# Kernel tuning notes

Measured on AMD Instinct MI355X. Metric: run time of the kernel, lower is better.

## Reference

```python
import math
import jax, jax.numpy as jnp
import numpy as np

D = 1024
H = 16
DK = D // H
B = 4
L = 2048


def setup_inputs() -> dict:
    key = jax.random.key(0)
    ks = jax.random.split(key, 11)
    s = 1.0 / math.sqrt(D)
    return {
        "q": jax.random.normal(ks[0], (B, L, D), jnp.float32),
        "k": jax.random.normal(ks[1], (B, L, D), jnp.float32),
        "v": jax.random.normal(ks[2], (B, L, D), jnp.float32),
        "wq_w": jax.random.normal(ks[3], (D, D), jnp.float32) * s,
        "wq_b": jnp.zeros((D,), jnp.float32),
        "wk_w": jax.random.normal(ks[4], (D, D), jnp.float32) * s,
        "wk_b": jnp.zeros((D,), jnp.float32),
        "wv_w": jax.random.normal(ks[5], (D, D), jnp.float32) * s,
        "wv_b": jnp.zeros((D,), jnp.float32),
        "wo_w": jax.random.normal(ks[6], (D, D), jnp.float32) * s,
        "wo_b": jnp.zeros((D,), jnp.float32),
    }


def reference(q, k, v, wq_w, wq_b, wk_w, wk_b, wv_w, wv_b, wo_w, wo_b):
    # torch Linear: x @ W.T + b
    Q = (q @ wq_w.T + wq_b).reshape(B, L, H, DK).transpose(0, 2, 1, 3)  # [B,H,L,DK]
    K = (k @ wk_w.T + wk_b).reshape(B, -1, H, DK).transpose(0, 2, 1, 3)
    V = (v @ wv_w.T + wv_b).reshape(B, -1, H, DK).transpose(0, 2, 1, 3)
    sc = jnp.einsum("bhqd,bhkd->bhqk", Q, K) / math.sqrt(DK)  # [B,H,L,L]
    # causal mask: strictly upper triangular filled with -1e9
    cm = jnp.triu(jnp.ones((L, L), dtype=bool), 1)
    sc = jnp.where(cm, jnp.float32(-1e9), sc)
    at = jax.nn.softmax(sc, axis=-1)  # dropout p=0 (eval)
    out = jnp.einsum("bhqk,bhkd->bhqd", at, V)  # [B,H,L,DK]
    out = out.transpose(0, 2, 1, 3).reshape(B, L, D)
    return out @ wo_w.T + wo_b
```

## Files before the change

kernel.cpp:

```cpp
#include <hip/hip_runtime.h>
#include <stdint.h>

#define DD 1024
#define NH 16
#define DHEAD 64
#define NB 4
#define SEQ 2048
#define MR (NB*SEQ)
#define NT (SEQ/128)

typedef __attribute__((ext_vector_type(8))) short s8v;
typedef __attribute__((ext_vector_type(4))) float f4v;

__device__ __forceinline__ unsigned short f2bf(float f) {
  union { float f; uint32_t u; } c; c.f = f;
  uint32_t u = c.u;
  u += 0x7fffu + ((u >> 16) & 1u);
  return (unsigned short)(u >> 16);
}
__device__ __forceinline__ unsigned short f2bf_trunc(float f) {
  union { float f; uint32_t u; } c; c.f = f;
  return (unsigned short)(c.u >> 16);
}

__device__ __forceinline__ void load_lds16(const void* g, void* lds) {
  __builtin_amdgcn_global_load_lds(
      (__attribute__((address_space(1))) void*)(uintptr_t)g,
      (__attribute__((address_space(3))) void*)(uint32_t)(uintptr_t)lds,
      16, 0, 0);
}

__global__ void cvt_all(
    const float* __restrict__ w0, const float* __restrict__ w1,
    const float* __restrict__ w2, const float* __restrict__ w3,
    const float* __restrict__ a0, const float* __restrict__ a1,
    const float* __restrict__ a2,
    unsigned short* __restrict__ dw0, unsigned short* __restrict__ dw1,
    unsigned short* __restrict__ dw2, unsigned short* __restrict__ dw3,
    unsigned short* __restrict__ da0, unsigned short* __restrict__ da1,
    unsigned short* __restrict__ da2)
{
  int blk = blockIdx.x;
  const float* src;
  unsigned short* dst;
  size_t i;
  if (blk < 2048) {
    int a = blk >> 9;
    src = a == 0 ? w0 : (a == 1 ? w1 : (a == 2 ? w2 : w3));
    dst = a == 0 ? dw0 : (a == 1 ? dw1 : (a == 2 ? dw2 : dw3));
    i = (size_t)(blk & 511) * 2048 + (size_t)threadIdx.x * 8;
  } else {
    int blk2 = blk - 2048;
    int a = blk2 >> 12;
    src = a == 0 ? a0 : (a == 1 ? a1 : a2);
    dst = a == 0 ? da0 : (a == 1 ? da1 : da2);
    i = (size_t)(blk2 & 4095) * 2048 + (size_t)threadIdx.x * 8;
  }
  float4 a4 = *(const float4*)(src + i);
  float4 b4 = *(const float4*)(src + i + 4);
  union { unsigned short us[8]; uint4 u; } t;
  t.us[0] = f2bf(a4.x); t.us[1] = f2bf(a4.y); t.us[2] = f2bf(a4.z); t.us[3] = f2bf(a4.w);
  t.us[4] = f2bf(b4.x); t.us[5] = f2bf(b4.y); t.us[6] = f2bf(b4.z); t.us[7] = f2bf(b4.w);
  *(uint4*)(dst + i) = t.u;
}

__global__ __launch_bounds__(256, 2) void gemm_bt(
    const unsigned short* __restrict__ A,
    const unsigned short* __restrict__ Bw,
    const float* __restrict__ bias,
    float* __restrict__ Cout)
{
  __shared__ __align__(16) short As[128 * 64];
  __shared__ __align__(16) short Bs[128 * 64];
  const int linear = blockIdx.y * 8 + blockIdx.x;
  const int nx = linear >> 6;
  const int my = linear & 63;
  const int tid = threadIdx.x;
  const int wave = tid >> 6, lane = tid & 63;
  const int wm = (wave >> 1) * 64, wn = (wave & 1) * 64;
  const int lr = lane & 15, lg = lane >> 4;
  const int sw = lr & 7;
  const unsigned short* Ab = A + (size_t)my * 128 * DD;
  const unsigned short* Bb = Bw + (size_t)nx * 128 * DD;

  f4v z = {0.f, 0.f, 0.f, 0.f};
  f4v acc[4][4];
  for (int mi = 0; mi < 4; mi++) for (int ni = 0; ni < 4; ni++) acc[mi][ni] = z;

  for (int k0 = 0; k0 < DD; k0 += 64) {
    __syncthreads();
    for (int i = 0; i < 4; i++) {
      int c = tid + i * 256;
      int row = c >> 3, pg = c & 7;
      load_lds16(Ab + (size_t)row * DD + k0 + ((pg ^ (row & 7)) << 3), As + c * 8);
    }
    for (int i = 0; i < 4; i++) {
      int c = tid + i * 256;
      int row = c >> 3, pg = c & 7;
      load_lds16(Bb + (size_t)row * DD + k0 + ((pg ^ (row & 7)) << 3), Bs + c * 8);
    }
    __syncthreads();
    for (int kk = 0; kk < 64; kk += 32) {
      int gb = kk >> 3;
      s8v af[4], bf[4];
      for (int i = 0; i < 4; i++)
        af[i] = *(const s8v*)(As + (wm + i * 16 + lr) * 64 + (((gb + lg) ^ sw) << 3));
      for (int i = 0; i < 4; i++)
        bf[i] = *(const s8v*)(Bs + (wn + i * 16 + lr) * 64 + (((gb + lg) ^ sw) << 3));
      for (int mi = 0; mi < 4; mi++)
        for (int ni = 0; ni < 4; ni++)
          acc[mi][ni] = __builtin_amdgcn_mfma_f32_16x16x32_bf16(af[mi], bf[ni], acc[mi][ni], 0, 0, 0);
    }
  }
  for (int ni = 0; ni < 4; ni++) {
    int col = nx * 128 + wn + ni * 16 + lr;
    float bv = bias[col];
    for (int mi = 0; mi < 4; mi++) {
      int row0 = my * 128 + wm + mi * 16 + lg * 4;
      for (int r = 0; r < 4; r++)
        Cout[(size_t)(row0 + r) * DD + col] = acc[mi][ni][r] + bv;
    }
  }
}

__global__ __launch_bounds__(256, 2) void gemm_qkv(
    const unsigned short* __restrict__ qA, const unsigned short* __restrict__ kA,
    const unsigned short* __restrict__ vA,
    const unsigned short* __restrict__ wq, const unsigned short* __restrict__ wk,
    const unsigned short* __restrict__ wv,
    const float* __restrict__ bq, const float* __restrict__ bk, const float* __restrict__ bv,
    unsigned short* __restrict__ Qp, unsigned short* __restrict__ Kp,
    unsigned short* __restrict__ VpT)
{
  __shared__ __align__(16) short As[128 * 64];
  __shared__ __align__(16) short Bs[128 * 64];
  const int linear = blockIdx.y * 24 + blockIdx.x;
  const int nx  = linear / 192;
  const int rem = linear % 192;
  const int seg = rem >> 6;
  const int my  = rem & 63;
  const unsigned short* A  = seg == 0 ? qA : (seg == 1 ? kA : vA);
  const unsigned short* Bw = seg == 0 ? wq : (seg == 1 ? wk : wv);
  const float* bias        = seg == 0 ? bq : (seg == 1 ? bk : bv);

  const int tid = threadIdx.x;
  const int wave = tid >> 6, lane = tid & 63;
  const int wm = (wave >> 1) * 64, wn = (wave & 1) * 64;
  const int lr = lane & 15, lg = lane >> 4;
  const int sw = lr & 7;
  const unsigned short* Ab = A + (size_t)my * 128 * DD;
  const unsigned short* Bb = Bw + (size_t)nx * 128 * DD;

  f4v z = {0.f, 0.f, 0.f, 0.f};
  f4v acc[4][4];
  for (int mi = 0; mi < 4; mi++) for (int ni = 0; ni < 4; ni++) acc[mi][ni] = z;

  for (int k0 = 0; k0 < DD; k0 += 64) {
    __syncthreads();
    for (int i = 0; i < 4; i++) {
      int c = tid + i * 256;
      int row = c >> 3, pg = c & 7;
      load_lds16(Ab + (size_t)row * DD + k0 + ((pg ^ (row & 7)) << 3), As + c * 8);
    }
    for (int i = 0; i < 4; i++) {
      int c = tid + i * 256;
      int row = c >> 3, pg = c & 7;
      load_lds16(Bb + (size_t)row * DD + k0 + ((pg ^ (row & 7)) << 3), Bs + c * 8);
    }
    __syncthreads();
    for (int kk = 0; kk < 64; kk += 32) {
      int gb = kk >> 3;
      s8v af[4], bf[4];
      for (int i = 0; i < 4; i++)
        af[i] = *(const s8v*)(As + (wm + i * 16 + lr) * 64 + (((gb + lg) ^ sw) << 3));
      for (int i = 0; i < 4; i++)
        bf[i] = *(const s8v*)(Bs + (wn + i * 16 + lr) * 64 + (((gb + lg) ^ sw) << 3));
      for (int mi = 0; mi < 4; mi++)
        for (int ni = 0; ni < 4; ni++)
          acc[mi][ni] = __builtin_amdgcn_mfma_f32_16x16x32_bf16(af[mi], bf[ni], acc[mi][ni], 0, 0, 0);
    }
  }
  if (seg < 2) {
    unsigned short* Cout = seg == 0 ? Qp : Kp;
    for (int ni = 0; ni < 4; ni++) {
      int col = nx * 128 + wn + ni * 16 + lr;
      float bv = bias[col];
      for (int mi = 0; mi < 4; mi++) {
        int row0 = my * 128 + wm + mi * 16 + lg * 4;
        for (int r = 0; r < 4; r++)
          Cout[(size_t)(row0 + r) * DD + col] = f2bf(acc[mi][ni][r] + bv);
      }
    }
  } else {
    for (int ni = 0; ni < 4; ni++) {
      int col = nx * 128 + wn + ni * 16 + lr;
      float bv = bias[col];
      int hh = col >> 6, dd = col & 63;
      for (int mi = 0; mi < 4; mi++) {
        int row0 = my * 128 + wm + mi * 16 + lg * 4;
        int bb = row0 >> 11, ll = row0 & 2047;
        uint64_t w = 0;
        for (int r = 0; r < 4; r++)
          w |= (uint64_t)f2bf(acc[mi][ni][r] + bv) << (16 * r);
        *(uint64_t*)(VpT + ((size_t)(bb * NH + hh) * 64 + dd) * SEQ + ll) = w;
      }
    }
  }
}

#define KS_STRIDE 72
#define VT_STRIDE 136
#define PS_STRIDE 72

__device__ __forceinline__ void attn_step(
    const s8v (&qf)[2][2], const s8v (&kf)[2][4],
    f4v (&o)[2][4], float (&ls)[2][4],
    int qbase, int colbase,
    const short* __restrict__ Vt, int vsub, short* __restrict__ Pw,
    int lr, int lg)
{
  const float csc = 0.125f * 1.44269504089f;
  const float FM = 14.0f;
  f4v zv = {0.f, 0.f, 0.f, 0.f};
  f4v s[2][4];
  for (int mi = 0; mi < 2; mi++) for (int ni = 0; ni < 4; ni++) s[mi][ni] = zv;
  __builtin_amdgcn_s_setprio(1);
  for (int ks = 0; ks < 2; ks++)
    for (int mi = 0; mi < 2; mi++)
      for (int ni = 0; ni < 4; ni++)
        s[mi][ni] = __builtin_amdgcn_mfma_f32_16x16x32_bf16(qf[mi][ks], kf[ks][ni], s[mi][ni], 0, 0, 0);
  __builtin_amdgcn_s_setprio(0);
  const bool diag = (colbase + 63 > qbase);
  for (int mi = 0; mi < 2; mi++)
    for (int ni = 0; ni < 4; ni++)
      for (int r = 0; r < 4; r++) {
        float e = __builtin_amdgcn_exp2f(fmaf(s[mi][ni][r], csc, -FM));
        if (diag) {
          int row = qbase + mi * 16 + lg * 4 + r;
          int col = colbase + ni * 16 + lr;
          e = (col > row) ? 0.f : e;
        }
        ls[mi][r] += e;
        Pw[(mi * 16 + lg * 4 + r) * PS_STRIDE + ni * 16 + lr] = (short)f2bf_trunc(e);
      }
  for (int kc2 = 0; kc2 < 2; kc2++) {
    s8v pf[2], vf[4];
    for (int mi = 0; mi < 2; mi++)
      pf[mi] = *(const s8v*)(Pw + (mi * 16 + lr) * PS_STRIDE + kc2 * 32 + lg * 8);
    for (int ni = 0; ni < 4; ni++)
      vf[ni] = *(const s8v*)(Vt + (ni * 16 + lr) * VT_STRIDE + vsub + kc2 * 32 + lg * 8);
    __builtin_amdgcn_s_setprio(1);
    for (int mi = 0; mi < 2; mi++)
      for (int ni = 0; ni < 4; ni++)
        o[mi][ni] = __builtin_amdgcn_mfma_f32_16x16x32_bf16(pf[mi], vf[ni], o[mi][ni], 0, 0, 0);
    __builtin_amdgcn_s_setprio(0);
  }
}

__global__ __launch_bounds__(256, 2) void fattn(
    const unsigned short* __restrict__ Qp,
    const unsigned short* __restrict__ Kp,
    const unsigned short* __restrict__ VpT,
    unsigned short* __restrict__ Op)
{
  __shared__ __align__(16) short Ks[128 * KS_STRIDE];
  __shared__ __align__(16) short Vt[64 * VT_STRIDE];
  __shared__ __align__(16) short Ps[8 * 32 * PS_STRIDE];
  const int tid = threadIdx.x;
  const int wave = tid >> 6, lane = tid & 63;
  const int lr = lane & 15, lg = lane >> 4;
  const int linear = blockIdx.y * 8 + blockIdx.x;
  const int xA = linear >> 6;
  const int bh = linear & 63;
  const int b = bh >> 4, h = bh & 15;
  const int xB = NT - 1 - xA;
  const int qbA = xA * 128 + wave * 32;
  const int qbB = xB * 128 + wave * 32;
  const unsigned short* Qrow = Qp + ((size_t)b * SEQ) * DD + h * DHEAD;
  const unsigned short* Krow = Kp + ((size_t)b * SEQ) * DD + h * DHEAD;
  const unsigned short* VT   = VpT + (size_t)bh * 64 * SEQ;
  short* PwB = Ps + wave * (64 * PS_STRIDE);
  short* PwA = PwB + 32 * PS_STRIDE;

  s8v qfA[2][2], qfB[2][2];
  for (int mi = 0; mi < 2; mi++)
    for (int ks = 0; ks < 2; ks++) {
      qfA[mi][ks] = *(const s8v*)(Qrow + (size_t)(qbA + mi * 16 + lr) * DD + ks * 32 + lg * 8);
      qfB[mi][ks] = *(const s8v*)(Qrow + (size_t)(qbB + mi * 16 + lr) * DD + ks * 32 + lg * 8);
    }

  f4v zv = {0.f, 0.f, 0.f, 0.f};
  f4v oA[2][4], oB[2][4];
  float lA[2][4], lB[2][4];
  for (int mi = 0; mi < 2; mi++)
    for (int r = 0; r < 4; r++) { lA[mi][r] = 0.f; lB[mi][r] = 0.f; }
  for (int mi = 0; mi < 2; mi++)
    for (int ni = 0; ni < 4; ni++) { oA[mi][ni] = zv; oB[mi][ni] = zv; }

  const int npair = xB + 1;

  int krow[4], kkc[4], vd[4], vkc[4];
  for (int i = 0; i < 4; i++) {
    int c = tid + i * 256;
    krow[i] = c >> 3; kkc[i] = (c & 7) << 3;
    vd[i] = c >> 4; vkc[i] = (c & 15) << 3;
  }
  s8v kreg[4], vreg[4];
  for (int i = 0; i < 4; i++) {
    kreg[i] = *(const s8v*)(Krow + (size_t)krow[i] * DD + kkc[i]);
    vreg[i] = *(const s8v*)(VT + (size_t)vd[i] * SEQ + vkc[i]);
  }

  for (int p = 0; p < npair; p++) {
    __syncthreads();
    for (int i = 0; i < 4; i++) {
      *(s8v*)(Ks + krow[i] * KS_STRIDE + kkc[i]) = kreg[i];
      *(s8v*)(Vt + vd[i] * VT_STRIDE + vkc[i]) = vreg[i];
    }
    __syncthreads();
    if (p + 1 < npair) {
      for (int i = 0; i < 4; i++) {
        kreg[i] = *(const s8v*)(Krow + (size_t)((p + 1) * 128 + krow[i]) * DD + kkc[i]);
        vreg[i] = *(const s8v*)(VT + (size_t)vd[i] * SEQ + (p + 1) * 128 + vkc[i]);
      }
    }
    for (int sub = 0; sub < 2; sub++) {
      int colbase = (2 * p + sub) * 64;
      bool actB = colbase <= qbB + 31;
      bool actA = colbase <= qbA + 31;
      if (actB || actA) {
        const short* KsSub = Ks + sub * 64 * KS_STRIDE;
        s8v kf[2][4];
        for (int ks = 0; ks < 2; ks++)
          for (int ni = 0; ni < 4; ni++)
            kf[ks][ni] = *(const s8v*)(KsSub + (ni * 16 + lr) * KS_STRIDE + ks * 32 + lg * 8);
        int vsub = sub * 64;
        if (actB) attn_step(qfB, kf, oB, lB, qbB, colbase, Vt, vsub, PwB, lr, lg);
        if (actA) attn_step(qfA, kf, oA, lA, qbA, colbase, Vt, vsub, PwA, lr, lg);
      }
    }
  }

  unsigned short* Orow = Op + ((size_t)b * SEQ) * DD + h * DHEAD;
  for (int mi = 0; mi < 2; mi++)
    for (int r = 0; r < 4; r++) {
      float sA = lA[mi][r], sB = lB[mi][r];
      for (int d2 = 1; d2 < 16; d2 <<= 1) {
        sA += __shfl_xor(sA, d2);
        sB += __shfl_xor(sB, d2);
      }
      float invA = 1.f / sA, invB = 1.f / sB;
      size_t rowA = (size_t)qbA + mi * 16 + lg * 4 + r;
      size_t rowB = (size_t)qbB + mi * 16 + lg * 4 + r;
      for (int ni = 0; ni < 4; ni++) {
        Orow[rowA * DD + ni * 16 + lr] = f2bf(oA[mi][ni][r] * invA);
        Orow[rowB * DD + ni * 16 + lr] = f2bf(oB[mi][ni][r] * invB);
      }
    }
}

extern "C" void kernel_launch(void* const* d_in, const int* in_sizes, int n_in,
                              void* d_out, int out_size, void* d_ws, size_t ws_size,
                              hipStream_t stream) {
  const float* q    = (const float*)d_in[0];
  const float* k    = (const float*)d_in[1];
  const float* v    = (const float*)d_in[2];
  const float* wq_w = (const float*)d_in[3];
  const float* wq_b = (const float*)d_in[4];
  const float* wk_w = (const float*)d_in[5];
  const float* wk_b = (const float*)d_in[6];
  const float* wv_w = (const float*)d_in[7];
  const float* wv_b = (const float*)d_in[8];
  const float* wo_w = (const float*)d_in[9];
  const float* wo_b = (const float*)d_in[10];

  const size_t BIG = (size_t)MR * DD;
  const size_t WSZ = (size_t)DD * DD;
  unsigned short* p = (unsigned short*)d_ws;
  unsigned short* wqb = p; p += WSZ;
  unsigned short* wkb = p; p += WSZ;
  unsigned short* wvb = p; p += WSZ;
  unsigned short* wob = p; p += WSZ;
  unsigned short* Qp  = p; p += BIG;
  unsigned short* Kp  = p; p += BIG;
  unsigned short* VpT = p; p += BIG;
  unsigned short* AO  = p; p += BIG;

  unsigned short* qb = AO;
  unsigned short* kb = (unsigned short*)d_out;
  unsigned short* vb = kb + BIG;

  cvt_all<<<dim3(14336), dim3(256), 0, stream>>>(
      wq_w, wk_w, wv_w, wo_w, q, k, v,
      wqb, wkb, wvb, wob, qb, kb, vb);

  gemm_qkv<<<dim3(24, MR / 128), dim3(256), 0, stream>>>(
      qb, kb, vb, wqb, wkb, wvb, wq_b, wk_b, wv_b, Qp, Kp, VpT);

  fattn<<<dim3(NT / 2, NB * NH), dim3(256), 0, stream>>>(Qp, Kp, VpT, AO);

  gemm_bt<<<dim3(8, MR / 128), dim3(256), 0, stream>>>(AO, wob, wo_b, (float*)d_out);

  (void)in_sizes; (void)n_in; (void)out_size; (void)ws_size;
}
```

Before: 321.6 us.

## Use 8 waves of 16 query rows per attention block, drop K/V prefetch

The attention kernel now runs 512 threads per block. Each wave owns 16 query rows per tile instead of 32, which halves the per-wave accumulators, Q fragments and P scratch. The register-held prefetch of the next K/V tile is removed, so loads are issued at the start of each iteration right before the barrier. The aim is to cut register pressure and raise occupancy to hide latency, at the cost of exposing global load latency and less K fragment reuse per wave.

New measurement: 329.1 us. 1.02x slower.

```diff
diff --git a/kernel.cpp b/kernel.cpp
--- a/kernel.cpp
+++ b/kernel.cpp
@@ -213,8 +213,8 @@
 #define PS_STRIDE 72
 
 __device__ __forceinline__ void attn_step(
-    const s8v (&qf)[2][2], const s8v (&kf)[2][4],
-    f4v (&o)[2][4], float (&ls)[2][4],
+    const s8v (&qf)[2], const s8v (&kf)[2][4],
+    f4v (&o)[4], float (&ls)[4],
     int qbase, int colbase,
     const short* __restrict__ Vt, int vsub, short* __restrict__ Pw,
     int lr, int lg)
@@ -222,42 +222,38 @@
   const float csc = 0.125f * 1.44269504089f;
   const float FM = 14.0f;
   f4v zv = {0.f, 0.f, 0.f, 0.f};
-  f4v s[2][4];
-  for (int mi = 0; mi < 2; mi++) for (int ni = 0; ni < 4; ni++) s[mi][ni] = zv;
+  f4v s[4];
+  for (int ni = 0; ni < 4; ni++) s[ni] = zv;
   __builtin_amdgcn_s_setprio(1);
   for (int ks = 0; ks < 2; ks++)
-    for (int mi = 0; mi < 2; mi++)
-      for (int ni = 0; ni < 4; ni++)
-        s[mi][ni] = __builtin_amdgcn_mfma_f32_16x16x32_bf16(qf[mi][ks], kf[ks][ni], s[mi][ni], 0, 0, 0);
+    for (int ni = 0; ni < 4; ni++)
+      s[ni] = __builtin_amdgcn_mfma_f32_16x16x32_bf16(qf[ks], kf[ks][ni], s[ni], 0, 0, 0);
   __builtin_amdgcn_s_setprio(0);
   const bool diag = (colbase + 63 > qbase);
-  for (int mi = 0; mi < 2; mi++)
-    for (int ni = 0; ni < 4; ni++)
-      for (int r = 0; r < 4; r++) {
-        float e = __builtin_amdgcn_exp2f(fmaf(s[mi][ni][r], csc, -FM));
-        if (diag) {
-          int row = qbase + mi * 16 + lg * 4 + r;
-          int col = colbase + ni * 16 + lr;
-          e = (col > row) ? 0.f : e;
-        }
-        ls[mi][r] += e;
-        Pw[(mi * 16 + lg * 4 + r) * PS_STRIDE + ni * 16 + lr] = (short)f2bf_trunc(e);
+  for (int ni = 0; ni < 4; ni++)
+    for (int r = 0; r < 4; r++) {
+      float e = __builtin_amdgcn_exp2f(fmaf(s[ni][r], csc, -FM));
+      if (diag) {
+        int row = qbase + lg * 4 + r;
+        int col = colbase + ni * 16 + lr;
+        e = (col > row) ? 0.f : e;
       }
+      ls[r] += e;
+      Pw[(lg * 4 + r) * PS_STRIDE + ni * 16 + lr] = (short)f2bf_trunc(e);
+    }
   for (int kc2 = 0; kc2 < 2; kc2++) {
-    s8v pf[2], vf[4];
-    for (int mi = 0; mi < 2; mi++)
-      pf[mi] = *(const s8v*)(Pw + (mi * 16 + lr) * PS_STRIDE + kc2 * 32 + lg * 8);
+    s8v pf, vf[4];
+    pf = *(const s8v*)(Pw + lr * PS_STRIDE + kc2 * 32 + lg * 8);
     for (int ni = 0; ni < 4; ni++)
       vf[ni] = *(const s8v*)(Vt + (ni * 16 + lr) * VT_STRIDE + vsub + kc2 * 32 + lg * 8);
     __builtin_amdgcn_s_setprio(1);
-    for (int mi = 0; mi < 2; mi++)
-      for (int ni = 0; ni < 4; ni++)
-        o[mi][ni] = __builtin_amdgcn_mfma_f32_16x16x32_bf16(pf[mi], vf[ni], o[mi][ni], 0, 0, 0);
+    for (int ni = 0; ni < 4; ni++)
+      o[ni] = __builtin_amdgcn_mfma_f32_16x16x32_bf16(pf, vf[ni], o[ni], 0, 0, 0);
     __builtin_amdgcn_s_setprio(0);
   }
 }
 
-__global__ __launch_bounds__(256, 2) void fattn(
+__global__ __launch_bounds__(512, 4) void fattn(
     const unsigned short* __restrict__ Qp,
     const unsigned short* __restrict__ Kp,
     const unsigned short* __restrict__ VpT,
@@ -265,7 +261,7 @@
 {
   __shared__ __align__(16) short Ks[128 * KS_STRIDE];
   __shared__ __align__(16) short Vt[64 * VT_STRIDE];
-  __shared__ __align__(16) short Ps[8 * 32 * PS_STRIDE];
+  __shared__ __align__(16) short Ps[8 * 16 * PS_STRIDE];
   const int tid = threadIdx.x;
   const int wave = tid >> 6, lane = tid & 63;
   const int lr = lane & 15, lg = lane >> 4;
@@ -274,60 +270,47 @@
   const int bh = linear & 63;
   const int b = bh >> 4, h = bh & 15;
   const int xB = NT - 1 - xA;
-  const int qbA = xA * 128 + wave * 32;
-  const int qbB = xB * 128 + wave * 32;
+  const int qbA = xA * 128 + wave * 16;
+  const int qbB = xB * 128 + wave * 16;
   const unsigned short* Qrow = Qp + ((size_t)b * SEQ) * DD + h * DHEAD;
   const unsigned short* Krow = Kp + ((size_t)b * SEQ) * DD + h * DHEAD;
   const unsigned short* VT   = VpT + (size_t)bh * 64 * SEQ;
-  short* PwB = Ps + wave * (64 * PS_STRIDE);
-  short* PwA = PwB + 32 * PS_STRIDE;
-
-  s8v qfA[2][2], qfB[2][2];
-  for (int mi = 0; mi < 2; mi++)
-    for (int ks = 0; ks < 2; ks++) {
-      qfA[mi][ks] = *(const s8v*)(Qrow + (size_t)(qbA + mi * 16 + lr) * DD + ks * 32 + lg * 8);
-      qfB[mi][ks] = *(const s8v*)(Qrow + (size_t)(qbB + mi * 16 + lr) * DD + ks * 32 + lg * 8);
-    }
+  short* Pw = Ps + wave * (16 * PS_STRIDE);
+
+  s8v qfA[2], qfB[2];
+  for (int ks = 0; ks < 2; ks++) {
+    qfA[ks] = *(const s8v*)(Qrow + (size_t)(qbA + lr) * DD + ks * 32 + lg * 8);
+    qfB[ks] = *(const s8v*)(Qrow + (size_t)(qbB + lr) * DD + ks * 32 + lg * 8);
+  }
 
   f4v zv = {0.f, 0.f, 0.f, 0.f};
-  f4v oA[2][4], oB[2][4];
-  float lA[2][4], lB[2][4];
-  for (int mi = 0; mi < 2; mi++)
-    for (int r = 0; r < 4; r++) { lA[mi][r] = 0.f; lB[mi][r] = 0.f; }
-  for (int mi = 0; mi < 2; mi++)
-    for (int ni = 0; ni < 4; ni++) { oA[mi][ni] = zv; oB[mi][ni] = zv; }
+  f4v oA[4], oB[4];
+  float lA[4], lB[4];
+  for (int r = 0; r < 4; r++) { lA[r] = 0.f; lB[r] = 0.f; }
+  for (int ni = 0; ni < 4; ni++) { oA[ni] = zv; oB[ni] = zv; }
 
   const int npair = xB + 1;
 
-  int krow[4], kkc[4], vd[4], vkc[4];
-  for (int i = 0; i < 4; i++) {
-    int c = tid + i * 256;
-    krow[i] = c >> 3; kkc[i] = (c & 7) << 3;
-    vd[i] = c >> 4; vkc[i] = (c & 15) << 3;
-  }
-  s8v kreg[4], vreg[4];
-  for (int i = 0; i < 4; i++) {
-    kreg[i] = *(const s8v*)(Krow + (size_t)krow[i] * DD + kkc[i]);
-    vreg[i] = *(const s8v*)(VT + (size_t)vd[i] * SEQ + vkc[i]);
-  }
-
   for (int p = 0; p < npair; p++) {
-    __syncthreads();
-    for (int i = 0; i < 4; i++) {
+    s8v kreg[2], vreg[2];
+    int krow[2], kkc[2], vd[2], vkc[2];
+    for (int i = 0; i < 2; i++) {
+      int c = tid + i * 512;
+      krow[i] = c >> 3; kkc[i] = (c & 7) << 3;
+      kreg[i] = *(const s8v*)(Krow + (size_t)(p * 128 + krow[i]) * DD + kkc[i]);
+      vd[i] = c >> 4; vkc[i] = (c & 15) << 3;
+      vreg[i] = *(const s8v*)(VT + (size_t)vd[i] * SEQ + p * 128 + vkc[i]);
+    }
+    __syncthreads();
+    for (int i = 0; i < 2; i++) {
       *(s8v*)(Ks + krow[i] * KS_STRIDE + kkc[i]) = kreg[i];
       *(s8v*)(Vt + vd[i] * VT_STRIDE + vkc[i]) = vreg[i];
     }
     __syncthreads();
-    if (p + 1 < npair) {
-      for (int i = 0; i < 4; i++) {
-        kreg[i] = *(const s8v*)(Krow + (size_t)((p + 1) * 128 + krow[i]) * DD + kkc[i]);
-        vreg[i] = *(const s8v*)(VT + (size_t)vd[i] * SEQ + (p + 1) * 128 + vkc[i]);
-      }
-    }
     for (int sub = 0; sub < 2; sub++) {
       int colbase = (2 * p + sub) * 64;
-      bool actB = colbase <= qbB + 31;
-      bool actA = colbase <= qbA + 31;
+      bool actB = colbase <= qbB + 15;
+      bool actA = colbase <= qbA + 15;
       if (actB || actA) {
         const short* KsSub = Ks + sub * 64 * KS_STRIDE;
         s8v kf[2][4];
@@ -335,28 +318,27 @@
           for (int ni = 0; ni < 4; ni++)
             kf[ks][ni] = *(const s8v*)(KsSub + (ni * 16 + lr) * KS_STRIDE + ks * 32 + lg * 8);
         int vsub = sub * 64;
-        if (actB) attn_step(qfB, kf, oB, lB, qbB, colbase, Vt, vsub, PwB, lr, lg);
-        if (actA) attn_step(qfA, kf, oA, lA, qbA, colbase, Vt, vsub, PwA, lr, lg);
+        if (actB) attn_step(qfB, kf, oB, lB, qbB, colbase, Vt, vsub, Pw, lr, lg);
+        if (actA) attn_step(qfA, kf, oA, lA, qbA, colbase, Vt, vsub, Pw, lr, lg);
       }
     }
   }
 
   unsigned short* Orow = Op + ((size_t)b * SEQ) * DD + h * DHEAD;
-  for (int mi = 0; mi < 2; mi++)
-    for (int r = 0; r < 4; r++) {
-      float sA = lA[mi][r], sB = lB[mi][r];
-      for (int d2 = 1; d2 < 16; d2 <<= 1) {
-        sA += __shfl_xor(sA, d2);
-        sB += __shfl_xor(sB, d2);
-      }
-      float invA = 1.f / sA, invB = 1.f / sB;
-      size_t rowA = (size_t)qbA + mi * 16 + lg * 4 + r;
-      size_t rowB = (size_t)qbB + mi * 16 + lg * 4 + r;
-      for (int ni = 0; ni < 4; ni++) {
-        Orow[rowA * DD + ni * 16 + lr] = f2bf(oA[mi][ni][r] * invA);
-        Orow[rowB * DD + ni * 16 + lr] = f2bf(oB[mi][ni][r] * invB);
-      }
-    }
+  for (int r = 0; r < 4; r++) {
+    float sA = lA[r], sB = lB[r];
+    for (int d2 = 1; d2 < 16; d2 <<= 1) {
+      sA += __shfl_xor(sA, d2);
+      sB += __shfl_xor(sB, d2);
+    }
+    float invA = 1.f / sA, invB = 1.f / sB;
+    size_t rowA = (size_t)qbA + lg * 4 + r;
+    size_t rowB = (size_t)qbB + lg * 4 + r;
+    for (int ni = 0; ni < 4; ni++) {
+      Orow[rowA * DD + ni * 16 + lr] = f2bf(oA[ni][r] * invA);
+      Orow[rowB * DD + ni * 16 + lr] = f2bf(oB[ni][r] * invB);
+    }
+  }
 }
 
 extern "C" void kernel_launch(void* const* d_in, const int* in_sizes, int n_in,
@@ -397,7 +379,7 @@
   gemm_qkv<<<dim3(24, MR / 128), dim3(256), 0, stream>>>(
       qb, kb, vb, wqb, wkb, wvb, wq_b, wk_b, wv_b, Qp, Kp, VpT);
 
-  fattn<<<dim3(NT / 2, NB * NH), dim3(256), 0, stream>>>(Qp, Kp, VpT, AO);
+  fattn<<<dim3(NT / 2, NB * NH), dim3(512), 0, stream>>>(Qp, Kp, VpT, AO);
 
   gemm_bt<<<dim3(8, MR / 128), dim3(256), 0, stream>>>(AO, wob, wo_b, (float*)d_out);
 
```

## Double-buffer GEMM LDS tiles and drop attention K/V register prefetch

Applied to the files above, without the earlier changes.

Both projection GEMMs (QKV and output) now keep two LDS buffers per operand. Tiles for step t+2 are issued with direct-to-LDS global loads while step t computes, with vmcnt waits and explicit barriers, so load latency overlaps the MFMA work. The attention kernel drops its register prefetch of the next K/V tile in favour of loading at the top of each iteration. It also shares one P scratch buffer between the two query tiles, cutting LDS use and register pressure, likely to raise occupancy at the cost of less load/compute overlap. The GEMM LDS footprint doubles to 64KB per block.

Measured after the change: 302.8 us. 1.06x faster.

```diff
diff --git a/kernel.cpp b/kernel.cpp
--- a/kernel.cpp
+++ b/kernel.cpp
@@ -8,6 +8,7 @@
 #define SEQ 2048
 #define MR (NB*SEQ)
 #define NT (SEQ/128)
+#define NKT (DD/64)
 
 typedef __attribute__((ext_vector_type(8))) short s8v;
 typedef __attribute__((ext_vector_type(4))) float f4v;
@@ -64,14 +65,54 @@
   *(uint4*)(dst + i) = t.u;
 }
 
+#define STAGE_AB(kt, bufi)                                                     \
+  for (int i_ = 0; i_ < 4; i_++) {                                             \
+    int c_ = tid + i_ * 256; int row_ = c_ >> 3, pg_ = c_ & 7;                 \
+    load_lds16(Ab + (size_t)row_ * DD + (kt) * 64 + ((pg_ ^ (row_ & 7)) << 3), \
+               &As[bufi][c_ * 8]);                                             \
+  }                                                                            \
+  for (int i_ = 0; i_ < 4; i_++) {                                             \
+    int c_ = tid + i_ * 256; int row_ = c_ >> 3, pg_ = c_ & 7;                 \
+    load_lds16(Bb + (size_t)row_ * DD + (kt) * 64 + ((pg_ ^ (row_ & 7)) << 3), \
+               &Bs[bufi][c_ * 8]);                                             \
+  }
+
+#define GEMM_KLOOP                                                             \
+  STAGE_AB(0, 0);                                                              \
+  STAGE_AB(1, 1);                                                              \
+  for (int t = 0; t < NKT; t++) {                                              \
+    if (t < NKT - 1) asm volatile("s_waitcnt vmcnt(8)" ::: "memory");          \
+    else             asm volatile("s_waitcnt vmcnt(0)" ::: "memory");          \
+    __builtin_amdgcn_sched_barrier(0);                                         \
+    __builtin_amdgcn_s_barrier();                                              \
+    __builtin_amdgcn_sched_barrier(0);                                         \
+    const short* Al = As[t & 1];                                               \
+    const short* Bl = Bs[t & 1];                                               \
+    for (int kk = 0; kk < 64; kk += 32) {                                      \
+      int gb = kk >> 3;                                                        \
+      s8v af[4], bf[4];                                                        \
+      for (int i = 0; i < 4; i++)                                              \
+        af[i] = *(const s8v*)(Al + (wm + i * 16 + lr) * 64 + (((gb + lg) ^ sw) << 3)); \
+      for (int i = 0; i < 4; i++)                                              \
+        bf[i] = *(const s8v*)(Bl + (wn + i * 16 + lr) * 64 + (((gb + lg) ^ sw) << 3)); \
+      for (int mi = 0; mi < 4; mi++)                                           \
+        for (int ni = 0; ni < 4; ni++)                                         \
+          acc[mi][ni] = __builtin_amdgcn_mfma_f32_16x16x32_bf16(af[mi], bf[ni], acc[mi][ni], 0, 0, 0); \
+    }                                                                          \
+    __builtin_amdgcn_sched_barrier(0);                                         \
+    __builtin_amdgcn_s_barrier();                                              \
+    __builtin_amdgcn_sched_barrier(0);                                         \
+    if (t + 2 < NKT) { STAGE_AB(t + 2, t & 1); }                               \
+  }
+
 __global__ __launch_bounds__(256, 2) void gemm_bt(
     const unsigned short* __restrict__ A,
     const unsigned short* __restrict__ Bw,
     const float* __restrict__ bias,
     float* __restrict__ Cout)
 {
-  __shared__ __align__(16) short As[128 * 64];
-  __shared__ __align__(16) short Bs[128 * 64];
+  __shared__ __align__(16) short As[2][128 * 64];
+  __shared__ __align__(16) short Bs[2][128 * 64];
   const int linear = blockIdx.y * 8 + blockIdx.x;
   const int nx = linear >> 6;
   const int my = linear & 63;
@@ -87,31 +128,8 @@
   f4v acc[4][4];
   for (int mi = 0; mi < 4; mi++) for (int ni = 0; ni < 4; ni++) acc[mi][ni] = z;
 
-  for (int k0 = 0; k0 < DD; k0 += 64) {
-    __syncthreads();
-    for (int i = 0; i < 4; i++) {
-      int c = tid + i * 256;
-      int row = c >> 3, pg = c & 7;
-      load_lds16(Ab + (size_t)row * DD + k0 + ((pg ^ (row & 7)) << 3), As + c * 8);
-    }
-    for (int i = 0; i < 4; i++) {
-      int c = tid + i * 256;
-      int row = c >> 3, pg = c & 7;
-      load_lds16(Bb + (size_t)row * DD + k0 + ((pg ^ (row & 7)) << 3), Bs + c * 8);
-    }
-    __syncthreads();
-    for (int kk = 0; kk < 64; kk += 32) {
-      int gb = kk >> 3;
-      s8v af[4], bf[4];
-      for (int i = 0; i < 4; i++)
-        af[i] = *(const s8v*)(As + (wm + i * 16 + lr) * 64 + (((gb + lg) ^ sw) << 3));
-      for (int i = 0; i < 4; i++)
-        bf[i] = *(const s8v*)(Bs + (wn + i * 16 + lr) * 64 + (((gb + lg) ^ sw) << 3));
-      for (int mi = 0; mi < 4; mi++)
-        for (int ni = 0; ni < 4; ni++)
-          acc[mi][ni] = __builtin_amdgcn_mfma_f32_16x16x32_bf16(af[mi], bf[ni], acc[mi][ni], 0, 0, 0);
-    }
-  }
+  GEMM_KLOOP
+
   for (int ni = 0; ni < 4; ni++) {
     int col = nx * 128 + wn + ni * 16 + lr;
     float bv = bias[col];
@@ -132,8 +150,8 @@
     unsigned short* __restrict__ Qp, unsigned short* __restrict__ Kp,
     unsigned short* __restrict__ VpT)
 {
-  __shared__ __align__(16) short As[128 * 64];
-  __shared__ __align__(16) short Bs[128 * 64];
+  __shared__ __align__(16) short As[2][128 * 64];
+  __shared__ __align__(16) short Bs[2][128 * 64];
   const int linear = blockIdx.y * 24 + blockIdx.x;
   const int nx  = linear / 192;
   const int rem = linear % 192;
@@ -155,31 +173,8 @@
   f4v acc[4][4];
   for (int mi = 0; mi < 4; mi++) for (int ni = 0; ni < 4; ni++) acc[mi][ni] = z;
 
-  for (int k0 = 0; k0 < DD; k0 += 64) {
-    __syncthreads();
-    for (int i = 0; i < 4; i++) {
-      int c = tid + i * 256;
-      int row = c >> 3, pg = c & 7;
-      load_lds16(Ab + (size_t)row * DD + k0 + ((pg ^ (row & 7)) << 3), As + c * 8);
-    }
-    for (int i = 0; i < 4; i++) {
-      int c = tid + i * 256;
-      int row = c >> 3, pg = c & 7;
-      load_lds16(Bb + (size_t)row * DD + k0 + ((pg ^ (row & 7)) << 3), Bs + c * 8);
-    }
-    __syncthreads();
-    for (int kk = 0; kk < 64; kk += 32) {
-      int gb = kk >> 3;
-      s8v af[4], bf[4];
-      for (int i = 0; i < 4; i++)
-        af[i] = *(const s8v*)(As + (wm + i * 16 + lr) * 64 + (((gb + lg) ^ sw) << 3));
-      for (int i = 0; i < 4; i++)
-        bf[i] = *(const s8v*)(Bs + (wn + i * 16 + lr) * 64 + (((gb + lg) ^ sw) << 3));
-      for (int mi = 0; mi < 4; mi++)
-        for (int ni = 0; ni < 4; ni++)
-          acc[mi][ni] = __builtin_amdgcn_mfma_f32_16x16x32_bf16(af[mi], bf[ni], acc[mi][ni], 0, 0, 0);
-    }
-  }
+  GEMM_KLOOP
+
   if (seg < 2) {
     unsigned short* Cout = seg == 0 ? Qp : Kp;
     for (int ni = 0; ni < 4; ni++) {
@@ -265,7 +260,7 @@
 {
   __shared__ __align__(16) short Ks[128 * KS_STRIDE];
   __shared__ __align__(16) short Vt[64 * VT_STRIDE];
-  __shared__ __align__(16) short Ps[8 * 32 * PS_STRIDE];
+  __shared__ __align__(16) short Ps[4 * 32 * PS_STRIDE];
   const int tid = threadIdx.x;
   const int wave = tid >> 6, lane = tid & 63;
   const int lr = lane & 15, lg = lane >> 4;
@@ -279,8 +274,7 @@
   const unsigned short* Qrow = Qp + ((size_t)b * SEQ) * DD + h * DHEAD;
   const unsigned short* Krow = Kp + ((size_t)b * SEQ) * DD + h * DHEAD;
   const unsigned short* VT   = VpT + (size_t)bh * 64 * SEQ;
-  short* PwB = Ps + wave * (64 * PS_STRIDE);
-  short* PwA = PwB + 32 * PS_STRIDE;
+  short* Pw = Ps + wave * (32 * PS_STRIDE);
 
   s8v qfA[2][2], qfB[2][2];
   for (int mi = 0; mi < 2; mi++)
@@ -299,31 +293,22 @@
 
   const int npair = xB + 1;
 
-  int krow[4], kkc[4], vd[4], vkc[4];
-  for (int i = 0; i < 4; i++) {
-    int c = tid + i * 256;
-    krow[i] = c >> 3; kkc[i] = (c & 7) << 3;
-    vd[i] = c >> 4; vkc[i] = (c & 15) << 3;
-  }
-  s8v kreg[4], vreg[4];
-  for (int i = 0; i < 4; i++) {
-    kreg[i] = *(const s8v*)(Krow + (size_t)krow[i] * DD + kkc[i]);
-    vreg[i] = *(const s8v*)(VT + (size_t)vd[i] * SEQ + vkc[i]);
-  }
-
   for (int p = 0; p < npair; p++) {
+    s8v kreg[4], vreg[4];
+    int krow[4], kkc[4], vd[4], vkc[4];
+    for (int i = 0; i < 4; i++) {
+      int c = tid + i * 256;
+      krow[i] = c >> 3; kkc[i] = (c & 7) << 3;
+      kreg[i] = *(const s8v*)(Krow + (size_t)(p * 128 + krow[i]) * DD + kkc[i]);
+      vd[i] = c >> 4; vkc[i] = (c & 15) << 3;
+      vreg[i] = *(const s8v*)(VT + (size_t)vd[i] * SEQ + p * 128 + vkc[i]);
+    }
     __syncthreads();
     for (int i = 0; i < 4; i++) {
       *(s8v*)(Ks + krow[i] * KS_STRIDE + kkc[i]) = kreg[i];
       *(s8v*)(Vt + vd[i] * VT_STRIDE + vkc[i]) = vreg[i];
     }
     __syncthreads();
-    if (p + 1 < npair) {
-      for (int i = 0; i < 4; i++) {
-        kreg[i] = *(const s8v*)(Krow + (size_t)((p + 1) * 128 + krow[i]) * DD + kkc[i]);
-        vreg[i] = *(const s8v*)(VT + (size_t)vd[i] * SEQ + (p + 1) * 128 + vkc[i]);
-      }
-    }
     for (int sub = 0; sub < 2; sub++) {
       int colbase = (2 * p + sub) * 64;
       bool actB = colbase <= qbB + 31;
@@ -335,8 +320,8 @@
           for (int ni = 0; ni < 4; ni++)
             kf[ks][ni] = *(const s8v*)(KsSub + (ni * 16 + lr) * KS_STRIDE + ks * 32 + lg * 8);
         int vsub = sub * 64;
-        if (actB) attn_step(qfB, kf, oB, lB, qbB, colbase, Vt, vsub, PwB, lr, lg);
-        if (actA) attn_step(qfA, kf, oA, lA, qbA, colbase, Vt, vsub, PwA, lr, lg);
+        if (actB) attn_step(qfB, kf, oB, lB, qbB, colbase, Vt, vsub, Pw, lr, lg);
+        if (actA) attn_step(qfA, kf, oA, lA, qbA, colbase, Vt, vsub, Pw, lr, lg);
       }
     }
   }
```
